# Kernel optimization log

Hardware: AMD Instinct MI355X
Metric: run time of the kernel (lower is better)

Reference implementation:

```python
import jax, jax.numpy as jnp
import numpy as np

B, T, E, A = 8, 2048, 1024, 1024


def setup_inputs() -> dict:
    key = jax.random.key(0)
    k1, k2, k3, k4 = jax.random.split(key, 4)
    embedded = jax.random.normal(k1, (B, T, E), dtype=jnp.float32)
    s = 1.0 / np.sqrt(E)
    # nn.Linear(E, A, bias=False) stores weight of shape (A, E); y = x @ W^T
    Wq = jax.random.uniform(k2, (A, E), dtype=jnp.float32, minval=-s, maxval=s)
    Wk = jax.random.uniform(k3, (A, E), dtype=jnp.float32, minval=-s, maxval=s)
    Wv = jax.random.uniform(k4, (A, E), dtype=jnp.float32, minval=-s, maxval=s)
    return {"embedded": embedded, "Wq": Wq, "Wk": Wk, "Wv": Wv}


def reference(embedded, Wq, Wk, Wv):
    # q, k, v: [B, T, A]
    q = jnp.einsum("bte,ae->bta", embedded, Wq)
    k = jnp.einsum("bte,ae->bta", embedded, Wk)
    v = jnp.einsum("bte,ae->bta", embedded, Wv)
    scale = 1.0 / jnp.sqrt(jnp.asarray(Wq.shape[0], dtype=q.dtype))
    # causal scores: [B, T, T]
    scores = jnp.einsum("bqa,bka->bqk", q, k) * scale
    t = scores.shape[-1]
    causal = jnp.tril(jnp.ones((t, t), dtype=bool))
    scores = jnp.where(causal, scores, jnp.asarray(-jnp.inf, dtype=scores.dtype))
    attn = jax.nn.softmax(scores, axis=-1)
    return jnp.einsum("bqk,bka->bqa", attn, v)
```

## Files before the change

kernel.cpp:

```cpp
#include <hip/hip_runtime.h>
#include <hip/hip_bf16.h>
#include <stdint.h>


#define BB 8
#define TT 2048
#define EE 1024
#define AA 1024
#define MM (BB * TT)

typedef short bf16x8 __attribute__((ext_vector_type(8)));
typedef float f32x4 __attribute__((ext_vector_type(4)));

#define GLOAD_LDS16(g, l)                                                      \
  __builtin_amdgcn_global_load_lds(                                            \
      (const __attribute__((address_space(1))) void*)(g),                      \
      (__attribute__((address_space(3))) void*)(l), 16, 0, 0)

#define SBAR()                               \
  do {                                       \
    __builtin_amdgcn_sched_barrier(0);       \
    __builtin_amdgcn_s_barrier();            \
    __builtin_amdgcn_sched_barrier(0);       \
  } while (0)

#define LGKM0()                                          \
  do {                                                   \
    asm volatile("s_waitcnt lgkmcnt(0)" ::: "memory");   \
    __builtin_amdgcn_sched_barrier(0);                   \
  } while (0)

#define VMCNT(n)                                              \
  do {                                                        \
    asm volatile("s_waitcnt vmcnt(" #n ")" ::: "memory");     \
    __builtin_amdgcn_sched_barrier(0);                        \
  } while (0)

__device__ __forceinline__ void gemm256_core(
    const short* __restrict__ gA, int lda, int a0row,
    const short* __restrict__ gB, int ldb, int b0row, int NT, short* As,
    short* Bs, f32x4 (*acc)[4]) {
  const int tid = threadIdx.x;
  const int lane = tid & 63;
  const int w = tid >> 6;
  const int wr = w >> 2, wc = w & 3;
  const int lrow = lane & 15;
  const int lk8 = (lane >> 4) * 8;
  const int swz = ((lrow >> 3) & 1) << 4;
  const int baseA = (((wr * 128 + lrow) * 32) + lk8) ^ swz;
  const int baseB = (((wc * 64 + lrow) * 32) + lk8) ^ swz;

  const short* pA[2];
  const short* pB[2];
  int dL[2];
#pragma unroll
  for (int i = 0; i < 2; ++i) {
    int chunk = 2 * w + i;
    int P = chunk * 1024 + lane * 16;
    int L = P ^ (((P >> 9) & 1) << 5);
    int row = L >> 6;
    int kb2 = (L & 63) >> 1;
    pA[i] = gA + (size_t)(a0row + row) * lda + kb2;
    pB[i] = gB + (size_t)(b0row + row) * ldb + kb2;
    dL[i] = chunk * 512 + lane * 8;
  }

#define STG_A(tl, s)                                                           \
  do {                                                                         \
    int _o = (tl) * 64 + (s) * 32;                                             \
    short* _d = As + (((tl) & 1) << 14) + ((s) << 13);                         \
    GLOAD_LDS16(pA[0] + _o, _d + dL[0]);                                       \
    GLOAD_LDS16(pA[1] + _o, _d + dL[1]);                                       \
  } while (0)
#define STG_B(tl, s)                                                           \
  do {                                                                         \
    int _o = (tl) * 64 + (s) * 32;                                             \
    short* _d = Bs + (((tl) & 1) << 14) + ((s) << 13);                         \
    GLOAD_LDS16(pB[0] + _o, _d + dL[0]);                                       \
    GLOAD_LDS16(pB[1] + _o, _d + dL[1]);                                       \
  } while (0)

  STG_B(0, 0); STG_A(0, 0); STG_B(0, 1); STG_A(0, 1);
  if (NT > 1) {
    STG_B(1, 0); STG_A(1, 0); STG_A(1, 1);
    VMCNT(6);
  } else {
    VMCNT(0);
  }
  SBAR();

  for (int t = 0; t < NT; ++t) {
    short* Ac = As + (t & 1) * 16384;
    short* Bc = Bs + (t & 1) * 16384;
    const bool stg = (t < NT - 2);
    bf16x8 a0[4], a1[4], a2[4], a3[4], b0[4], b1[4];

#pragma unroll
    for (int m = 0; m < 4; ++m) a0[m] = *(const bf16x8*)&Ac[baseA + m * 512];
#pragma unroll
    for (int n = 0; n < 4; ++n) b0[n] = *(const bf16x8*)&Bc[baseB + n * 512];
    if (t < NT - 1) STG_B(t + 1, 1);
    SBAR();
    LGKM0();
    __builtin_amdgcn_s_setprio(1);
#pragma unroll
    for (int m = 0; m < 4; ++m)
#pragma unroll
      for (int n = 0; n < 4; ++n)
        acc[m][n] = __builtin_amdgcn_mfma_f32_16x16x32_bf16(a0[m], b0[n],
                                                            acc[m][n], 0, 0, 0);
    __builtin_amdgcn_s_setprio(0);
    SBAR();

#pragma unroll
    for (int m = 0; m < 4; ++m)
      a1[m] = *(const bf16x8*)&Ac[baseA + (m + 4) * 512];
#pragma unroll
    for (int m = 0; m < 4; ++m)
      a2[m] = *(const bf16x8*)&Ac[8192 + baseA + m * 512];
    if (stg) STG_B(t + 2, 0);
    SBAR();
    LGKM0();
    __builtin_amdgcn_s_setprio(1);
#pragma unroll
    for (int m = 0; m < 4; ++m)
#pragma unroll
      for (int n = 0; n < 4; ++n)
        acc[m + 4][n] = __builtin_amdgcn_mfma_f32_16x16x32_bf16(
            a1[m], b0[n], acc[m + 4][n], 0, 0, 0);
    __builtin_amdgcn_s_setprio(0);
    SBAR();

#pragma unroll
    for (int m = 0; m < 4; ++m)
      a3[m] = *(const bf16x8*)&Ac[8192 + baseA + (m + 4) * 512];
#pragma unroll
    for (int n = 0; n < 4; ++n)
      b1[n] = *(const bf16x8*)&Bc[8192 + baseB + n * 512];
    if (stg) STG_A(t + 2, 0);
    SBAR();
    LGKM0();
    __builtin_amdgcn_s_setprio(1);
#pragma unroll
    for (int m = 0; m < 4; ++m)
#pragma unroll
      for (int n = 0; n < 4; ++n)
        acc[m][n] = __builtin_amdgcn_mfma_f32_16x16x32_bf16(a2[m], b1[n],
                                                            acc[m][n], 0, 0, 0);
    __builtin_amdgcn_s_setprio(0);
    SBAR();

    if (stg) {
      STG_A(t + 2, 1);
      VMCNT(6);
    } else if (t == NT - 2) {
      VMCNT(0);
    }
    SBAR();
    __builtin_amdgcn_s_setprio(1);
#pragma unroll
    for (int m = 0; m < 4; ++m)
#pragma unroll
      for (int n = 0; n < 4; ++n)
        acc[m + 4][n] = __builtin_amdgcn_mfma_f32_16x16x32_bf16(
            a3[m], b1[n], acc[m + 4][n], 0, 0, 0);
    __builtin_amdgcn_s_setprio(0);
    SBAR();
  }
#undef STG_A
#undef STG_B
}

__device__ __forceinline__ void stage_tile(const short* __restrict__ g,
                                           size_t stride, short* lds, int tid) {
#pragma unroll
  for (int r = 0; r < 4; ++r) {
    int t = r * 256 + tid;
    int row = t >> 3;
    int c = (t & 7) * 8;
    GLOAD_LDS16(g + (size_t)row * stride + c, lds + (size_t)t * 8);
  }
}

__device__ __forceinline__ void mfma_step(const short* As, const short* Bs,
                                          f32x4 acc[4][4], int lane, int wr,
                                          int wc) {
  int lrow = lane & 15;
  int lk = (lane >> 4) * 8;
#pragma unroll
  for (int kk = 0; kk < 64; kk += 32) {
    bf16x8 a[4], b[4];
#pragma unroll
    for (int i = 0; i < 4; ++i)
      a[i] = *(const bf16x8*)&As[(wr * 64 + i * 16 + lrow) * 64 + kk + lk];
#pragma unroll
    for (int j = 0; j < 4; ++j)
      b[j] = *(const bf16x8*)&Bs[(wc * 64 + j * 16 + lrow) * 64 + kk + lk];
#pragma unroll
    for (int i = 0; i < 4; ++i)
#pragma unroll
      for (int j = 0; j < 4; ++j)
        acc[i][j] =
            __builtin_amdgcn_mfma_f32_16x16x32_bf16(a[i], b[j], acc[i][j], 0, 0, 0);
  }
}

__global__ __launch_bounds__(512, 2) void qkv_qk(
    const short* __restrict__ xb, const short* __restrict__ Wb,
    short* __restrict__ qk) {
  __shared__ __align__(16) short SH[65536];
  short* As = SH;
  short* Bs = SH + 32768;
  int f = blockIdx.x;
  int s = (f & 7) * 64 + (f >> 3);
  int mt = s >> 3;
  int rem = s & 7;
  int z = rem >> 2, ntl = rem & 3;
  const short* gB = Wb + (size_t)z * AA * EE + (size_t)(ntl * 256) * EE;
  f32x4 acc[8][4];
#pragma unroll
  for (int m = 0; m < 8; ++m)
#pragma unroll
    for (int n = 0; n < 4; ++n) acc[m][n] = (f32x4){0.f, 0.f, 0.f, 0.f};
  gemm256_core(xb, EE, mt * 256, gB, EE, 0, EE / 64, As, Bs, acc);

  int tid = threadIdx.x;
  int lane = tid & 63, w = tid >> 6, wr = w >> 2, wc = w & 3;
  int lrow = lane & 15, lk4 = (lane >> 4) * 4;
  short* o = qk + (size_t)z * MM * AA;
  int row0 = mt * 256 + wr * 128;
  int col0 = ntl * 256 + wc * 64;
#pragma unroll
  for (int m = 0; m < 8; ++m)
#pragma unroll
    for (int n = 0; n < 4; ++n)
#pragma unroll
      for (int r = 0; r < 4; ++r) {
        int row = row0 + m * 16 + lk4 + r;
        int col = col0 + n * 16 + lrow;
        __hip_bfloat16 h = __float2bfloat16(acc[m][n][r]);
        o[(size_t)row * AA + col] = *(short*)&h;
      }
}

__global__ __launch_bounds__(512, 2) void score_v(
    const short* __restrict__ xb, const short* __restrict__ Wb,
    const short* __restrict__ Qb, const short* __restrict__ Kb,
    short* __restrict__ Pu, float* __restrict__ lsum,
    short* __restrict__ Vt) {
  __shared__ __align__(16) short SH[65536];
  short* As = SH;
  short* Bs = SH + 32768;
  int f = blockIdx.x;
  int tid = threadIdx.x;
  int lane = tid & 63, w = tid >> 6, wr8 = w >> 2, wc8 = w & 3;
  int lrow = lane & 15, lk4 = (lane >> 4) * 4;
  const float scale = 0.03125f;

  if (f < 224) {
    int b = f & 7;
    int j = f >> 3;
    int MT = 1;
    while ((MT + 1) * MT / 2 <= j) ++MT;
    int NT = j - MT * (MT - 1) / 2;
    const short* Q = Qb + (size_t)b * TT * AA;
    const short* K = Kb + (size_t)b * TT * AA;
    short* P = Pu + (size_t)b * TT * TT;

    {
      f32x4 acc[8][4];
#pragma unroll
      for (int m = 0; m < 8; ++m)
#pragma unroll
        for (int n = 0; n < 4; ++n) acc[m][n] = (f32x4){0.f, 0.f, 0.f, 0.f};
      gemm256_core(Q, AA, MT * 256, K, AA, NT * 256, AA / 64, As, Bs, acc);

      int q0 = MT * 256 + wr8 * 128;
      int c0 = NT * 256 + wc8 * 64;
#pragma unroll
      for (int m = 0; m < 8; ++m) {
#pragma unroll
        for (int r = 0; r < 4; ++r) {
          int q = q0 + m * 16 + lk4 + r;
          float rs = 0.f;
#pragma unroll
          for (int n = 0; n < 4; ++n) {
            int kx = c0 + n * 16 + lrow;
            float e = __expf(acc[m][n][r] * scale);
            rs += e;
            __hip_bfloat16 h = __float2bfloat16(e);
            P[(size_t)q * TT + kx] = *(short*)&h;
          }
          rs += __shfl_xor(rs, 1);
          rs += __shfl_xor(rs, 2);
          rs += __shfl_xor(rs, 4);
          rs += __shfl_xor(rs, 8);
          if (lrow == 0) atomicAdd(&lsum[b * TT + q], rs);
        }
      }
    }

    if (j < 24) {
      int M = j / 3, r3 = j - 3 * M;
      int mt = 2 * M + (r3 > 0);
      int nt = 2 * M + (r3 == 2);
      int q0 = mt * 128, c0 = nt * 128;
      bool act = tid < 256;
      int wid4 = (tid >> 6) & 3, wr = wid4 >> 1, wc = wid4 & 1;

      f32x4 acc[4][4];
#pragma unroll
      for (int i = 0; i < 4; ++i)
#pragma unroll
        for (int jj = 0; jj < 4; ++jj) acc[i][jj] = (f32x4){0.f, 0.f, 0.f, 0.f};

      __syncthreads();
      for (int k0 = 0; k0 < AA; k0 += 64) {
        if (act) {
          stage_tile(Q + (size_t)q0 * AA + k0, AA, As, tid);
          stage_tile(K + (size_t)c0 * AA + k0, AA, Bs, tid);
        }
        __syncthreads();
        if (act) mfma_step(As, Bs, acc, lane, wr, wc);
        __syncthreads();
      }
      if (act) {
#pragma unroll
        for (int i = 0; i < 4; ++i) {
#pragma unroll
          for (int r = 0; r < 4; ++r) {
            int q = q0 + wr * 64 + i * 16 + lk4 + r;
            float rs = 0.f;
#pragma unroll
            for (int jj = 0; jj < 4; ++jj) {
              int kx = c0 + wc * 64 + jj * 16 + lrow;
              float e = (kx <= q) ? __expf(acc[i][jj][r] * scale) : 0.f;
              rs += e;
              __hip_bfloat16 h = __float2bfloat16(e);
              P[(size_t)q * TT + kx] = *(short*)&h;
            }
            rs += __shfl_xor(rs, 1);
            rs += __shfl_xor(rs, 2);
            rs += __shfl_xor(rs, 4);
            rs += __shfl_xor(rs, 8);
            if (lrow == 0) atomicAdd(&lsum[b * TT + q], rs);
          }
        }
      }
    }
  } else {
    int g = f - 224;
    int s2 = (g & 7) * 32 + (g >> 3);
    int mt = s2 >> 2, ntl = s2 & 3;
    const short* gB = Wb + (size_t)2 * AA * EE + (size_t)(ntl * 256) * EE;
    f32x4 acc[8][4];
#pragma unroll
    for (int m = 0; m < 8; ++m)
#pragma unroll
      for (int n = 0; n < 4; ++n) acc[m][n] = (f32x4){0.f, 0.f, 0.f, 0.f};
    gemm256_core(xb, EE, mt * 256, gB, EE, 0, EE / 64, As, Bs, acc);

    __syncthreads();
    int lr0 = wr8 * 128, lc0 = wc8 * 64;
#pragma unroll
    for (int m = 0; m < 8; ++m)
#pragma unroll
      for (int n = 0; n < 4; ++n)
#pragma unroll
        for (int r = 0; r < 4; ++r) {
          int lr = lr0 + m * 16 + lk4 + r;
          int lc = lc0 + n * 16 + lrow;
          __hip_bfloat16 h = __float2bfloat16(acc[m][n][r]);
          SH[lc * 256 + (lr ^ ((lc & 7) << 3))] = *(short*)&h;
        }
    __syncthreads();
    int row0 = mt * 256;
    int bq = row0 >> 11;
    int t0 = row0 & 2047;
#pragma unroll
    for (int pass = 0; pass < 4; ++pass) {
      int lc = pass * 64 + (tid >> 3);
      int d = ntl * 256 + lc;
      size_t dst = ((size_t)bq * AA + d) * TT + t0;
      int sw = (lc & 7) << 3;
#pragma unroll
      for (int gg = 0; gg < 4; ++gg) {
        int lr = (tid & 7) * 8 + gg * 64;
        bf16x8 vv = *(const bf16x8*)&SH[lc * 256 + (lr ^ sw)];
        *(bf16x8*)&Vt[dst + lr] = vv;
      }
    }
  }
}

__global__ __launch_bounds__(256) void pv_gemm(const short* __restrict__ Pu,
                                               const short* __restrict__ Vt,
                                               const float* __restrict__ lsum,
                                               float* __restrict__ out) {
  int f = blockIdx.x;
  int b = f & 7;
  int j = f >> 3;
  int p = j >> 3;
  int nt = j & 7;
  int n0 = nt * 128;

  __shared__ __align__(16) short As[128 * 64];
  __shared__ __align__(16) short Bs[128 * 64];
  int tid = threadIdx.x;
  int lane = tid & 63, wid = tid >> 6, wr = wid >> 1, wc = wid & 1;
  const short* P = Pu + (size_t)b * TT * TT;
  const short* V = Vt + (size_t)b * AA * TT;
  int lrow = lane & 15, lk4 = (lane >> 4) * 4;

#pragma unroll
  for (int s = 0; s < 2; ++s) {
    int mt = s ? (15 - p) : p;
    int q0 = mt * 128;
    f32x4 acc[4][4];
#pragma unroll
    for (int i = 0; i < 4; ++i)
#pragma unroll
      for (int jj = 0; jj < 4; ++jj) acc[i][jj] = (f32x4){0.f, 0.f, 0.f, 0.f};

    int kend = q0 + 128;
    for (int k0 = 0; k0 < kend; k0 += 64) {
      stage_tile(P + (size_t)q0 * TT + k0, TT, As, tid);
      stage_tile(V + (size_t)n0 * TT + k0, TT, Bs, tid);
      __syncthreads();
      mfma_step(As, Bs, acc, lane, wr, wc);
      __syncthreads();
    }
#pragma unroll
    for (int i = 0; i < 4; ++i) {
#pragma unroll
      for (int r = 0; r < 4; ++r) {
        int q = q0 + wr * 64 + i * 16 + lk4 + r;
        float linv = 1.0f / lsum[b * TT + q];
#pragma unroll
        for (int jj = 0; jj < 4; ++jj) {
          int d = n0 + wc * 64 + jj * 16 + lrow;
          out[((size_t)(b * TT + q)) * AA + d] = acc[i][jj][r] * linv;
        }
      }
    }
  }
}

__global__ void prep(const float* __restrict__ x, const float* __restrict__ wq,
                     const float* __restrict__ wk, const float* __restrict__ wv,
                     short* __restrict__ Xb, short* __restrict__ Wb,
                     float* __restrict__ Ls) {
  const int nx4 = MM * EE / 4;
  const int nw4 = AA * EE / 4;
  int gid = blockIdx.x * blockDim.x + threadIdx.x;
  if (gid < MM) Ls[gid] = 0.f;
  int stride = gridDim.x * blockDim.x;
  for (int i = gid; i < nx4 + 3 * nw4; i += stride) {
    const float* src;
    short* dst;
    int ii;
    if (i < nx4) {
      src = x; dst = Xb; ii = i;
    } else {
      int j = i - nx4;
      int z = j / nw4;
      ii = j - z * nw4;
      src = (z == 0) ? wq : (z == 1 ? wk : wv);
      dst = Wb + (size_t)z * AA * EE;
    }
    float4 v = ((const float4*)src)[ii];
    __hip_bfloat16 h0 = __float2bfloat16(v.x);
    __hip_bfloat16 h1 = __float2bfloat16(v.y);
    __hip_bfloat16 h2 = __float2bfloat16(v.z);
    __hip_bfloat16 h3 = __float2bfloat16(v.w);
    short4 o;
    o.x = *(short*)&h0;
    o.y = *(short*)&h1;
    o.z = *(short*)&h2;
    o.w = *(short*)&h3;
    ((short4*)dst)[ii] = o;
  }
}

extern "C" void kernel_launch(void* const* d_in, const int* in_sizes, int n_in,
                              void* d_out, int out_size, void* d_ws,
                              size_t ws_size, hipStream_t stream) {
  const float* x = (const float*)d_in[0];
  const float* Wq = (const float*)d_in[1];
  const float* Wk = (const float*)d_in[2];
  const float* Wv = (const float*)d_in[3];

  char* ws = (char*)d_ws;
  size_t oWb = 0;
  size_t oQb = oWb + (size_t)3 * AA * EE * 2;
  size_t oKb = oQb + (size_t)MM * AA * 2;
  size_t oVt = oKb + (size_t)MM * AA * 2;
  size_t oLs = oVt + (size_t)MM * AA * 2;
  size_t oXb = oLs + (size_t)MM * 4;
  size_t oPu = oXb + (size_t)MM * EE * 2;

  short* Wb = (short*)(ws + oWb);
  short* Qb = (short*)(ws + oQb);
  short* Kb = (short*)(ws + oKb);
  short* Vt = (short*)(ws + oVt);
  float* Ls = (float*)(ws + oLs);
  short* Xb = (short*)(ws + oXb);
  short* Pu = (short*)(ws + oPu);

  prep<<<2048, 256, 0, stream>>>(x, Wq, Wk, Wv, Xb, Wb, Ls);

  qkv_qk<<<512, 512, 0, stream>>>(Xb, Wb, Qb);
  score_v<<<480, 512, 0, stream>>>(Xb, Wb, Qb, Kb, Pu, Ls, Vt);
  pv_gemm<<<512, 256, 0, stream>>>(Pu, Vt, Ls, (float*)d_out);
}
```

Before: 244.8 us.

## Widen PV GEMM tile to 256 columns with 512-thread blocks

```diff
diff --git a/kernel.cpp b/kernel.cpp
--- a/kernel.cpp
+++ b/kernel.cpp
@@ -393,28 +393,28 @@
   }
 }
 
-__global__ __launch_bounds__(256) void pv_gemm(const short* __restrict__ Pu,
+__global__ __launch_bounds__(512) void pv_gemm(const short* __restrict__ Pu,
                                                const short* __restrict__ Vt,
                                                const float* __restrict__ lsum,
                                                float* __restrict__ out) {
   int f = blockIdx.x;
   int b = f & 7;
   int j = f >> 3;
-  int p = j >> 3;
-  int nt = j & 7;
-  int n0 = nt * 128;
-
-  __shared__ __align__(16) short As[128 * 64];
-  __shared__ __align__(16) short Bs[128 * 64];
+  int pp = j >> 2;
+  int nt = j & 3;
+  int n0 = nt * 256;
+
+  __shared__ __align__(16) short Ps[128 * 64];
+  __shared__ __align__(16) short Vs[256 * 64];
   int tid = threadIdx.x;
-  int lane = tid & 63, wid = tid >> 6, wr = wid >> 1, wc = wid & 1;
+  int lane = tid & 63, w = tid >> 6, wq = w >> 2, wd = w & 3;
   const short* P = Pu + (size_t)b * TT * TT;
   const short* V = Vt + (size_t)b * AA * TT;
   int lrow = lane & 15, lk4 = (lane >> 4) * 4;
 
 #pragma unroll
   for (int s = 0; s < 2; ++s) {
-    int mt = s ? (15 - p) : p;
+    int mt = s ? (15 - pp) : pp;
     int q0 = mt * 128;
     f32x4 acc[4][4];
 #pragma unroll
@@ -424,21 +424,33 @@
 
     int kend = q0 + 128;
     for (int k0 = 0; k0 < kend; k0 += 64) {
-      stage_tile(P + (size_t)q0 * TT + k0, TT, As, tid);
-      stage_tile(V + (size_t)n0 * TT + k0, TT, Bs, tid);
+#pragma unroll
+      for (int r = 0; r < 2; ++r) {
+        int t = r * 512 + tid;
+        int row = t >> 3;
+        int c = (t & 7) * 8;
+        GLOAD_LDS16(P + (size_t)(q0 + row) * TT + k0 + c, Ps + (size_t)t * 8);
+      }
+#pragma unroll
+      for (int r = 0; r < 4; ++r) {
+        int t = r * 512 + tid;
+        int row = t >> 3;
+        int c = (t & 7) * 8;
+        GLOAD_LDS16(V + (size_t)(n0 + row) * TT + k0 + c, Vs + (size_t)t * 8);
+      }
       __syncthreads();
-      mfma_step(As, Bs, acc, lane, wr, wc);
+      mfma_step(Ps, Vs, acc, lane, wq, wd);
       __syncthreads();
     }
 #pragma unroll
     for (int i = 0; i < 4; ++i) {
 #pragma unroll
       for (int r = 0; r < 4; ++r) {
-        int q = q0 + wr * 64 + i * 16 + lk4 + r;
+        int q = q0 + wq * 64 + i * 16 + lk4 + r;
         float linv = 1.0f / lsum[b * TT + q];
 #pragma unroll
         for (int jj = 0; jj < 4; ++jj) {
-          int d = n0 + wc * 64 + jj * 16 + lrow;
+          int d = n0 + wd * 64 + jj * 16 + lrow;
           out[((size_t)(b * TT + q)) * AA + d] = acc[i][jj][r] * linv;
         }
       }
@@ -511,5 +523,5 @@
 
   qkv_qk<<<512, 512, 0, stream>>>(Xb, Wb, Qb);
   score_v<<<480, 512, 0, stream>>>(Xb, Wb, Qb, Kb, Pu, Ls, Vt);
-  pv_gemm<<<512, 256, 0, stream>>>(Pu, Vt, Ls, (float*)d_out);
-}
+  pv_gemm<<<256, 512, 0, stream>>>(Pu, Vt, Ls, (float*)d_out);
+}
```

Result: slower. 252.3 us (+3.0%).

## Distribute diagonal score tiles via atomic work-stealing counter across all blocks

Applied to the files above, without the earlier changes.

```diff
diff --git a/kernel.cpp b/kernel.cpp
--- a/kernel.cpp
+++ b/kernel.cpp
@@ -247,8 +247,9 @@
     const short* __restrict__ xb, const short* __restrict__ Wb,
     const short* __restrict__ Qb, const short* __restrict__ Kb,
     short* __restrict__ Pu, float* __restrict__ lsum,
-    short* __restrict__ Vt) {
+    short* __restrict__ Vt, int* __restrict__ Dc) {
   __shared__ __align__(16) short SH[65536];
+  __shared__ int steal_idx;
   short* As = SH;
   short* Bs = SH + 32768;
   int f = blockIdx.x;
@@ -267,85 +268,34 @@
     const short* K = Kb + (size_t)b * TT * AA;
     short* P = Pu + (size_t)b * TT * TT;
 
-    {
-      f32x4 acc[8][4];
-#pragma unroll
-      for (int m = 0; m < 8; ++m)
-#pragma unroll
-        for (int n = 0; n < 4; ++n) acc[m][n] = (f32x4){0.f, 0.f, 0.f, 0.f};
-      gemm256_core(Q, AA, MT * 256, K, AA, NT * 256, AA / 64, As, Bs, acc);
-
-      int q0 = MT * 256 + wr8 * 128;
-      int c0 = NT * 256 + wc8 * 64;
-#pragma unroll
-      for (int m = 0; m < 8; ++m) {
-#pragma unroll
-        for (int r = 0; r < 4; ++r) {
-          int q = q0 + m * 16 + lk4 + r;
-          float rs = 0.f;
-#pragma unroll
-          for (int n = 0; n < 4; ++n) {
-            int kx = c0 + n * 16 + lrow;
-            float e = __expf(acc[m][n][r] * scale);
-            rs += e;
-            __hip_bfloat16 h = __float2bfloat16(e);
-            P[(size_t)q * TT + kx] = *(short*)&h;
-          }
-          rs += __shfl_xor(rs, 1);
-          rs += __shfl_xor(rs, 2);
-          rs += __shfl_xor(rs, 4);
-          rs += __shfl_xor(rs, 8);
-          if (lrow == 0) atomicAdd(&lsum[b * TT + q], rs);
+    f32x4 acc[8][4];
+#pragma unroll
+    for (int m = 0; m < 8; ++m)
+#pragma unroll
+      for (int n = 0; n < 4; ++n) acc[m][n] = (f32x4){0.f, 0.f, 0.f, 0.f};
+    gemm256_core(Q, AA, MT * 256, K, AA, NT * 256, AA / 64, As, Bs, acc);
+
+    int q0 = MT * 256 + wr8 * 128;
+    int c0 = NT * 256 + wc8 * 64;
+#pragma unroll
+    for (int m = 0; m < 8; ++m) {
+#pragma unroll
+      for (int r = 0; r < 4; ++r) {
+        int q = q0 + m * 16 + lk4 + r;
+        float rs = 0.f;
+#pragma unroll
+        for (int n = 0; n < 4; ++n) {
+          int kx = c0 + n * 16 + lrow;
+          float e = __expf(acc[m][n][r] * scale);
+          rs += e;
+          __hip_bfloat16 h = __float2bfloat16(e);
+          P[(size_t)q * TT + kx] = *(short*)&h;
         }
-      }
-    }
-
-    if (j < 24) {
-      int M = j / 3, r3 = j - 3 * M;
-      int mt = 2 * M + (r3 > 0);
-      int nt = 2 * M + (r3 == 2);
-      int q0 = mt * 128, c0 = nt * 128;
-      bool act = tid < 256;
-      int wid4 = (tid >> 6) & 3, wr = wid4 >> 1, wc = wid4 & 1;
-
-      f32x4 acc[4][4];
-#pragma unroll
-      for (int i = 0; i < 4; ++i)
-#pragma unroll
-        for (int jj = 0; jj < 4; ++jj) acc[i][jj] = (f32x4){0.f, 0.f, 0.f, 0.f};
-
-      __syncthreads();
-      for (int k0 = 0; k0 < AA; k0 += 64) {
-        if (act) {
-          stage_tile(Q + (size_t)q0 * AA + k0, AA, As, tid);
-          stage_tile(K + (size_t)c0 * AA + k0, AA, Bs, tid);
-        }
-        __syncthreads();
-        if (act) mfma_step(As, Bs, acc, lane, wr, wc);
-        __syncthreads();
-      }
-      if (act) {
-#pragma unroll
-        for (int i = 0; i < 4; ++i) {
-#pragma unroll
-          for (int r = 0; r < 4; ++r) {
-            int q = q0 + wr * 64 + i * 16 + lk4 + r;
-            float rs = 0.f;
-#pragma unroll
-            for (int jj = 0; jj < 4; ++jj) {
-              int kx = c0 + wc * 64 + jj * 16 + lrow;
-              float e = (kx <= q) ? __expf(acc[i][jj][r] * scale) : 0.f;
-              rs += e;
-              __hip_bfloat16 h = __float2bfloat16(e);
-              P[(size_t)q * TT + kx] = *(short*)&h;
-            }
-            rs += __shfl_xor(rs, 1);
-            rs += __shfl_xor(rs, 2);
-            rs += __shfl_xor(rs, 4);
-            rs += __shfl_xor(rs, 8);
-            if (lrow == 0) atomicAdd(&lsum[b * TT + q], rs);
-          }
-        }
+        rs += __shfl_xor(rs, 1);
+        rs += __shfl_xor(rs, 2);
+        rs += __shfl_xor(rs, 4);
+        rs += __shfl_xor(rs, 8);
+        if (lrow == 0) atomicAdd(&lsum[b * TT + q], rs);
       }
     }
   } else {
@@ -391,6 +341,64 @@
       }
     }
   }
+
+  bool act = tid < 256;
+  int wid4 = (tid >> 6) & 3, wrd = wid4 >> 1, wcd = wid4 & 1;
+  for (;;) {
+    __syncthreads();
+    if (tid == 0) steal_idx = atomicAdd(Dc, 1);
+    __syncthreads();
+    int idx = steal_idx;
+    if (idx >= 192) break;
+    int b2 = idx / 24;
+    int j2 = idx - b2 * 24;
+    int M = j2 / 3, r3 = j2 - 3 * M;
+    int mt = 2 * M + (r3 > 0);
+    int nt = 2 * M + (r3 == 2);
+    int q0 = mt * 128, c0 = nt * 128;
+    const short* Q = Qb + (size_t)b2 * TT * AA;
+    const short* K = Kb + (size_t)b2 * TT * AA;
+    short* P = Pu + (size_t)b2 * TT * TT;
+
+    f32x4 acc[4][4];
+#pragma unroll
+    for (int i = 0; i < 4; ++i)
+#pragma unroll
+      for (int jj = 0; jj < 4; ++jj) acc[i][jj] = (f32x4){0.f, 0.f, 0.f, 0.f};
+
+    for (int k0 = 0; k0 < AA; k0 += 64) {
+      if (act) {
+        stage_tile(Q + (size_t)q0 * AA + k0, AA, As, tid);
+        stage_tile(K + (size_t)c0 * AA + k0, AA, Bs, tid);
+      }
+      __syncthreads();
+      if (act) mfma_step(As, Bs, acc, lane, wrd, wcd);
+      __syncthreads();
+    }
+    if (act) {
+#pragma unroll
+      for (int i = 0; i < 4; ++i) {
+#pragma unroll
+        for (int r = 0; r < 4; ++r) {
+          int q = q0 + wrd * 64 + i * 16 + lk4 + r;
+          float rs = 0.f;
+#pragma unroll
+          for (int jj = 0; jj < 4; ++jj) {
+            int kx = c0 + wcd * 64 + jj * 16 + lrow;
+            float e = (kx <= q) ? __expf(acc[i][jj][r] * scale) : 0.f;
+            rs += e;
+            __hip_bfloat16 h = __float2bfloat16(e);
+            P[(size_t)q * TT + kx] = *(short*)&h;
+          }
+          rs += __shfl_xor(rs, 1);
+          rs += __shfl_xor(rs, 2);
+          rs += __shfl_xor(rs, 4);
+          rs += __shfl_xor(rs, 8);
+          if (lrow == 0) atomicAdd(&lsum[b2 * TT + q], rs);
+        }
+      }
+    }
+  }
 }
 
 __global__ __launch_bounds__(256) void pv_gemm(const short* __restrict__ Pu,
@@ -449,11 +457,12 @@
 __global__ void prep(const float* __restrict__ x, const float* __restrict__ wq,
                      const float* __restrict__ wk, const float* __restrict__ wv,
                      short* __restrict__ Xb, short* __restrict__ Wb,
-                     float* __restrict__ Ls) {
+                     float* __restrict__ Ls, int* __restrict__ Dc) {
   const int nx4 = MM * EE / 4;
   const int nw4 = AA * EE / 4;
   int gid = blockIdx.x * blockDim.x + threadIdx.x;
   if (gid < MM) Ls[gid] = 0.f;
+  if (gid == 0) Dc[0] = 0;
   int stride = gridDim.x * blockDim.x;
   for (int i = gid; i < nx4 + 3 * nw4; i += stride) {
     const float* src;
@@ -496,7 +505,8 @@
   size_t oKb = oQb + (size_t)MM * AA * 2;
   size_t oVt = oKb + (size_t)MM * AA * 2;
   size_t oLs = oVt + (size_t)MM * AA * 2;
-  size_t oXb = oLs + (size_t)MM * 4;
+  size_t oDc = oLs + (size_t)MM * 4;
+  size_t oXb = oDc + 256;
   size_t oPu = oXb + (size_t)MM * EE * 2;
 
   short* Wb = (short*)(ws + oWb);
@@ -504,12 +514,13 @@
   short* Kb = (short*)(ws + oKb);
   short* Vt = (short*)(ws + oVt);
   float* Ls = (float*)(ws + oLs);
+  int* Dc = (int*)(ws + oDc);
   short* Xb = (short*)(ws + oXb);
   short* Pu = (short*)(ws + oPu);
 
-  prep<<<2048, 256, 0, stream>>>(x, Wq, Wk, Wv, Xb, Wb, Ls);
+  prep<<<2048, 256, 0, stream>>>(x, Wq, Wk, Wv, Xb, Wb, Ls, Dc);
 
   qkv_qk<<<512, 512, 0, stream>>>(Xb, Wb, Qb);
-  score_v<<<480, 512, 0, stream>>>(Xb, Wb, Qb, Kb, Pu, Ls, Vt);
+  score_v<<<480, 512, 0, stream>>>(Xb, Wb, Qb, Kb, Pu, Ls, Vt, Dc);
   pv_gemm<<<512, 256, 0, stream>>>(Pu, Vt, Ls, (float*)d_out);
 }
```

New measurement: 254.5 us. 3.9% more time.
